# Performance work log

Measured on AMD Instinct MI355X. Metric: run time of the kernel, lower is better.

Reference implementation:

```python
import jax, jax.numpy as jnp
import numpy as np

D_MODEL, D_K, D_V, H, D_FF = 512, 64, 64, 8, 2048
B, N = 8, 1024
LN_EPS = 1e-5


def _layer_norm(x, g, b):
    mu = jnp.mean(x, axis=-1, keepdims=True)
    var = jnp.mean((x - mu) ** 2, axis=-1, keepdims=True)
    return (x - mu) * jax.lax.rsqrt(var + LN_EPS) * g + b


def setup_inputs() -> dict:
    key = jax.random.key(0)
    ks = jax.random.split(key, 16)
    s = 0.02
    return {
        "queries": jax.random.normal(ks[0], (B, N, D_MODEL), jnp.float32),
        "keys": jax.random.normal(ks[1], (B, N, D_MODEL), jnp.float32),
        "values": jax.random.normal(ks[2], (B, N, D_MODEL), jnp.float32),
        "relative_geometry_weights": jax.random.uniform(ks[3], (B, H, N, N), jnp.float32),
        "pos": jax.random.normal(ks[4], (B, N, D_MODEL), jnp.float32),
        "Wq": jax.random.normal(ks[5], (D_MODEL, H * D_K), jnp.float32) * s,
        "bq": jnp.zeros((H * D_K,), jnp.float32),
        "Wk": jax.random.normal(ks[6], (D_MODEL, H * D_K), jnp.float32) * s,
        "bk": jnp.zeros((H * D_K,), jnp.float32),
        "Wv": jax.random.normal(ks[7], (D_MODEL, H * D_V), jnp.float32) * s,
        "bv": jnp.zeros((H * D_V,), jnp.float32),
        "Wo": jax.random.normal(ks[8], (H * D_V, D_MODEL), jnp.float32) * s,
        "bo": jnp.zeros((D_MODEL,), jnp.float32),
        "ln1_g": jnp.ones((D_MODEL,), jnp.float32),
        "ln1_b": jnp.zeros((D_MODEL,), jnp.float32),
        "W1": jax.random.normal(ks[9], (D_MODEL, D_FF), jnp.float32) * s,
        "b1": jnp.zeros((D_FF,), jnp.float32),
        "W2": jax.random.normal(ks[10], (D_FF, D_MODEL), jnp.float32) * s,
        "b2": jnp.zeros((D_MODEL,), jnp.float32),
        "ln2_g": jnp.ones((D_MODEL,), jnp.float32),
        "ln2_b": jnp.zeros((D_MODEL,), jnp.float32),
    }


def reference(queries, keys, values, relative_geometry_weights, pos,
              Wq, bq, Wk, bk, Wv, bv, Wo, bo, ln1_g, ln1_b,
              W1, b1, W2, b2, ln2_g, ln2_b):
    b, n, _ = queries.shape
    # positional injection on q/k only
    q_in = queries + pos
    k_in = keys + pos
    # projections -> [b, h, n, d]
    q = (q_in @ Wq + bq).reshape(b, n, H, D_K).transpose(0, 2, 1, 3)
    k = (k_in @ Wk + bk).reshape(b, n, H, D_K).transpose(0, 2, 1, 3)
    v = (values @ Wv + bv).reshape(b, n, H, D_V).transpose(0, 2, 1, 3)
    # scaled dot-product scores with geometry bias: log(clamp(w_g)) + scores
    att = jnp.einsum('bhqd,bhkd->bhqk', q, k) / jnp.sqrt(jnp.float32(D_K))
    w_mn = jnp.log(jnp.clip(relative_geometry_weights, 1e-6, None)) + att
    w_mn = jax.nn.softmax(w_mn, axis=-1)
    out = jnp.einsum('bhqk,bhkd->bhqd', w_mn, v)  # [b,h,n,d_v]
    out = out.transpose(0, 2, 1, 3).reshape(b, n, H * D_V) @ Wo + bo
    # residual + layernorm (dropout is identity in eval)
    att_out = _layer_norm(queries + out, ln1_g, ln1_b)
    # position-wise FFN with residual + layernorm
    ff = jax.nn.relu(att_out @ W1 + b1) @ W2 + b2
    return _layer_norm(att_out + ff, ln2_g, ln2_b)
```

## Files before the change

kernel.cpp:

```cpp
#include <hip/hip_runtime.h>
#include <hip/hip_bf16.h>
#include <stdint.h>

#define B_   8
#define N_   1024
#define DM   512
#define H_   8
#define DFF  2048
#define ROWS (B_ * N_)
#define QKV_LD (3 * DM)
#define LOG2E 1.4426950408889634f
#define SCL  (0.125f * LOG2E)

typedef __bf16 bf16x8 __attribute__((ext_vector_type(8)));
typedef float  f32x4  __attribute__((ext_vector_type(4)));

__device__ __forceinline__ void gld_lds16(const void* g, void* l) {
  __builtin_amdgcn_global_load_lds((__attribute__((address_space(1))) void*)g,
                                   (__attribute__((address_space(3))) void*)l, 16, 0, 0);
}

__device__ __forceinline__ unsigned short bfb(float x) {
  __bf16 h = (__bf16)x;
  unsigned short u;
  __builtin_memcpy(&u, &h, 2);
  return u;
}

__global__ __launch_bounds__(256) void prep_x(
    const float* __restrict__ q, const float* __restrict__ k,
    const float* __restrict__ v, const float* __restrict__ pos,
    __bf16* __restrict__ xq, __bf16* __restrict__ xk, __bf16* __restrict__ xv) {
  int i = blockIdx.x * 256 + threadIdx.x;
  float4 pv = ((const float4*)pos)[i];
  float4 qv = ((const float4*)q)[i];
  float4 kv = ((const float4*)k)[i];
  float4 vv = ((const float4*)v)[i];
  ushort4 o;
  o.x = bfb(qv.x + pv.x); o.y = bfb(qv.y + pv.y); o.z = bfb(qv.z + pv.z); o.w = bfb(qv.w + pv.w);
  ((ushort4*)xq)[i] = o;
  o.x = bfb(kv.x + pv.x); o.y = bfb(kv.y + pv.y); o.z = bfb(kv.z + pv.z); o.w = bfb(kv.w + pv.w);
  ((ushort4*)xk)[i] = o;
  o.x = bfb(vv.x); o.y = bfb(vv.y); o.z = bfb(vv.z); o.w = bfb(vv.w);
  ((ushort4*)xv)[i] = o;
}

__global__ __launch_bounds__(256) void transpose_all(
    const float* __restrict__ Wq, const float* __restrict__ Wk,
    const float* __restrict__ Wv, const float* __restrict__ Wo,
    const float* __restrict__ W1, const float* __restrict__ W2,
    __bf16* __restrict__ WqkvT, __bf16* __restrict__ WoT,
    __bf16* __restrict__ W1T, __bf16* __restrict__ W2T) {
  __shared__ float tl[32][33];
  int idx = blockIdx.x;
  const float* src; __bf16* dst; int K, N, t;
  if (idx < 768) {
    src = idx < 256 ? Wq : (idx < 512 ? Wk : Wv);
    dst = WqkvT + (size_t)(idx >> 8) * 512 * 512;
    K = 512; N = 512; t = idx & 255;
  } else if (idx < 1024) { src = Wo; dst = WoT;  K = 512;  N = 512;  t = idx - 768; }
  else if (idx < 2048)   { src = W1; dst = W1T;  K = 512;  N = 2048; t = idx - 1024; }
  else                   { src = W2; dst = W2T;  K = 2048; N = 512;  t = idx - 2048; }
  int tiles_n = N >> 5;
  int tn = t & (tiles_n - 1), tk = t / tiles_n;
  int n0 = tn * 32, k0 = tk * 32;
  int x = threadIdx.x & 31, y4 = threadIdx.x >> 5;
  #pragma unroll
  for (int j = y4; j < 32; j += 8) tl[j][x] = src[(size_t)(k0 + j) * N + n0 + x];
  __syncthreads();
  #pragma unroll
  for (int j = y4; j < 32; j += 8)
    dst[(size_t)(n0 + j) * K + k0 + x] = (__bf16)tl[x][j];
}

__global__ __launch_bounds__(256) void transpose_v(
    const __bf16* __restrict__ QKV, __bf16* __restrict__ Vt) {
  __shared__ __bf16 t[32][33];
  int bh = blockIdx.y;
  int b = bh >> 3, h = bh & 7;
  int tn = blockIdx.x >> 1;
  int td = blockIdx.x & 1;
  int x = threadIdx.x & 31, y4 = threadIdx.x >> 5;
  #pragma unroll
  for (int j = y4; j < 32; j += 8)
    t[j][x] = QKV[(size_t)(b * N_ + tn * 32 + j) * QKV_LD + 2 * DM + h * 64 + td * 32 + x];
  __syncthreads();
  #pragma unroll
  for (int j = y4; j < 32; j += 8)
    Vt[(size_t)(bh * 64 + td * 32 + j) * N_ + tn * 32 + x] = t[x][j];
}

template <int EPI, int BN>
__global__ __launch_bounds__(256, 2) void gemm_bt(
    const __bf16* __restrict__ A0, const __bf16* __restrict__ A1, const __bf16* __restrict__ A2,
    const __bf16* __restrict__ BT,
    const float* __restrict__ bias0, const float* __restrict__ bias1, const float* __restrict__ bias2,
    void* __restrict__ Cp, int M, int N, int K, int nsplit) {
  constexpr int NFR = BN / 32;
  constexpr int WCW = BN / 2;
  constexpr int BI  = BN / 32;
  __shared__ __align__(16) __bf16 As[128 * 64];
  __shared__ __align__(16) __bf16 Bs[BN * 64];
  int tid = threadIdx.x, lane = tid & 63;
  int wave = tid >> 6;
  int wr = (wave >> 1) * 64, wc = (wave & 1) * WCW;

  int gx = N / BN;
  int nwg = gridDim.x;
  int cpx = nwg >> 3;
  int swz = (blockIdx.x & 7) * cpx + (blockIdx.x >> 3);
  int bx = swz % gx, by = swz / gx;
  int row0 = by << 7, col0 = bx * BN;

  int asel = col0 / nsplit;
  const __bf16* A = asel == 0 ? A0 : (asel == 1 ? A1 : A2);
  const float* bias = asel == 0 ? bias0 : (asel == 1 ? bias1 : bias2);

  f32x4 acc[4][NFR] = {};

  for (int kt = 0; kt < K; kt += 64) {
    #pragma unroll
    for (int i = 0; i < 4; ++i) {
      int t = i * 256 + tid;
      int r = t >> 3, cL = t & 7;
      int cS = cL ^ (r & 7);
      gld_lds16(A + (size_t)(row0 + r) * K + kt + cS * 8, As + t * 8);
    }
    #pragma unroll
    for (int i = 0; i < BI; ++i) {
      int t = i * 256 + tid;
      int r = t >> 3, cL = t & 7;
      int cS = cL ^ (r & 7);
      gld_lds16(BT + (size_t)(col0 + r) * K + kt + cS * 8, Bs + t * 8);
    }
    __syncthreads();
    #pragma unroll
    for (int ks = 0; ks < 2; ++ks) {
      bf16x8 af[4], bfr[NFR];
      #pragma unroll
      for (int m = 0; m < 4; ++m) {
        int r = wr + m * 16 + (lane & 15);
        int c = (ks * 4 + (lane >> 4)) ^ (r & 7);
        af[m] = *(const bf16x8*)(As + r * 64 + c * 8);
      }
      #pragma unroll
      for (int n = 0; n < NFR; ++n) {
        int r = wc + n * 16 + (lane & 15);
        int c = (ks * 4 + (lane >> 4)) ^ (r & 7);
        bfr[n] = *(const bf16x8*)(Bs + r * 64 + c * 8);
      }
      #pragma unroll
      for (int m = 0; m < 4; ++m)
        #pragma unroll
        for (int n = 0; n < NFR; ++n)
          acc[m][n] = __builtin_amdgcn_mfma_f32_16x16x32_bf16(af[m], bfr[n], acc[m][n], 0, 0, 0);
    }
    __syncthreads();
  }

  int rb = row0 + wr + ((lane >> 4) << 2);
  int cb = col0 + wc + (lane & 15);
  #pragma unroll
  for (int n = 0; n < NFR; ++n) {
    int c = cb + n * 16;
    float bv = bias[c % nsplit];
    #pragma unroll
    for (int m = 0; m < 4; ++m) {
      #pragma unroll
      for (int j = 0; j < 4; ++j) {
        int r = rb + m * 16 + j;
        float v = acc[m][n][j] + bv;
        if (EPI == 1) v = fmaxf(v, 0.f);
        if (EPI == 2) ((float*)Cp)[(size_t)r * N + c] = v;
        else          ((__bf16*)Cp)[(size_t)r * N + c] = (__bf16)v;
      }
    }
  }
}

__global__ __launch_bounds__(256, 3) void attn_kernel(
    const __bf16* __restrict__ QKV, const __bf16* __restrict__ Vt,
    const float* __restrict__ rgw, __bf16* __restrict__ O) {
  __shared__ __align__(16) __bf16 Qs[64 * 64];
  __shared__ __align__(16) __bf16 Ks[2][64 * 64];
  __shared__ __align__(16) __bf16 Vs[2][64 * 64];
  __shared__ __align__(16) __bf16 Ps[4][16 * 64];

  int tid = threadIdx.x, lane = tid & 63, wave = tid >> 6;
  int flat = (blockIdx.x & 7) * 128 + (blockIdx.x >> 3);
  int qt = flat & 15, h = (flat >> 4) & 7, b = flat >> 7;
  int q0 = qt * 64;
  const int g = lane >> 4, u = lane & 15;

  const float* rgw_p = rgw +
      ((size_t)(b * H_ + h) * N_ + (size_t)(q0 + wave * 16 + u)) * N_ + g * 4;

#define STAGE_KV(BUF, KT)                                                      \
  {                                                                            \
    _Pragma("unroll")                                                          \
    for (int i = 0; i < 2; ++i) {                                              \
      int t = i * 256 + tid;                                                   \
      int r = t >> 3, cL = t & 7, cS = cL ^ (r & 7);                           \
      gld_lds16(QKV + (size_t)(b * N_ + (KT) + r) * QKV_LD + DM + h * 64 + cS * 8, Ks[BUF] + t * 8); \
      gld_lds16(Vt + (size_t)((b * H_ + h) * 64 + r) * N_ + (KT) + cS * 8, Vs[BUF] + t * 8);         \
    }                                                                          \
  }

  #pragma unroll
  for (int i = 0; i < 2; ++i) {
    int t = i * 256 + tid;
    int r = t >> 3, cL = t & 7, cS = cL ^ (r & 7);
    gld_lds16(QKV + (size_t)(b * N_ + q0 + r) * QKV_LD + h * 64 + cS * 8, Qs + t * 8);
  }
  STAGE_KV(0, 0)
  __builtin_amdgcn_sched_barrier(0);
  f32x4 wA[4], wB[4];
  #pragma unroll
  for (int n = 0; n < 4; ++n) wA[n] = *(const f32x4*)(rgw_p + n * 16);
  #pragma unroll
  for (int n = 0; n < 4; ++n) wB[n] = *(const f32x4*)(rgw_p + 64 + n * 16);

  float l = 0.f;
  f32x4 oacc[4] = {};
  bf16x8 qf[2];
  __bf16* pw = &Ps[wave][0];

  union Pk { __bf16 h4[4]; unsigned long long q; };

#define PHASE(T16, CUR, WC, DOSTAGE, DOPF, WAITSTR)                            \
  {                                                                            \
    asm volatile(WAITSTR ::: "memory");                                        \
    __builtin_amdgcn_s_barrier();                                              \
    if (DOSTAGE) { STAGE_KV((CUR) ^ 1, ((T16) + 1) * 64) }                     \
    __builtin_amdgcn_sched_barrier(0);      \
    if ((T16) == 0) {                                                          \
      int r = wave * 16 + u;                                                   \
      _Pragma("unroll")                                                        \
      for (int ks = 0; ks < 2; ++ks) {                                         \
        int c = (ks * 4 + g) ^ (r & 7);                                        \
        qf[ks] = *(const bf16x8*)(Qs + r * 64 + c * 8);                        \
      }                                                                        \
    }                                                                          \
                        \
    f32x4 s[4] = {};                                                           \
    __builtin_amdgcn_s_setprio(1);                                             \
    _Pragma("unroll")                                                          \
    for (int ks = 0; ks < 2; ++ks) {                                           \
      _Pragma("unroll")                                                        \
      for (int n = 0; n < 4; ++n) {                                            \
        int r = n * 16 + u;                                                    \
        int c = (ks * 4 + g) ^ (r & 7);                                        \
        bf16x8 kf = *(const bf16x8*)(Ks[CUR] + r * 64 + c * 8);                \
        s[n] = __builtin_amdgcn_mfma_f32_16x16x32_bf16(kf, qf[ks], s[n], 0, 0, 0); \
      }                                                                        \
    }                                                                          \
    __builtin_amdgcn_s_setprio(0);                                             \
                           \
    _Pragma("unroll")                                                          \
    for (int n = 0; n < 4; ++n) {                                              \
      Pk pk;                                                                   \
      _Pragma("unroll")                                                        \
      for (int j = 0; j < 4; ++j) {                                            \
        float pv = fmaxf(WC[n][j], 1e-6f) * exp2f(s[n][j] * SCL);              \
        l += pv;                                                               \
        pk.h4[j] = (__bf16)pv;                                                 \
      }                                                                        \
      int bcol = 2 * n + (g >> 1);                                             \
      *(unsigned long long*)(pw + u * 64 + ((bcol ^ (u & 7)) << 3) + ((g & 1) << 2)) = pk.q; \
    }                                                                          \
    if (DOPF) {                                                                \
      _Pragma("unroll")                                                        \
      for (int n = 0; n < 4; ++n)                                              \
        WC[n] = *(const f32x4*)(rgw_p + ((T16) + 2) * 64 + n * 16);            \
    }                                                                          \
                                                               \
    __builtin_amdgcn_s_setprio(1);                                             \
    _Pragma("unroll")                                                          \
    for (int ks = 0; ks < 2; ++ks) {                                           \
      int cp = (ks * 4 + g) ^ (u & 7);                                         \
      bf16x8 pa = *(const bf16x8*)(pw + u * 64 + cp * 8);                      \
      _Pragma("unroll")                                                        \
      for (int n = 0; n < 4; ++n) {                                            \
        int r = n * 16 + u;                                                    \
        int c = (ks * 4 + g) ^ (r & 7);                                        \
        bf16x8 vb = *(const bf16x8*)(Vs[CUR] + r * 64 + c * 8);                \
        oacc[n] = __builtin_amdgcn_mfma_f32_16x16x32_bf16(pa, vb, oacc[n], 0, 0, 0); \
      }                                                                        \
    }                                                                          \
    __builtin_amdgcn_s_setprio(0);                                             \
  }

  PHASE(0, 0, wA, 1, 1, "s_waitcnt vmcnt(4)")
  PHASE(1, 1, wB, 1, 1, "s_waitcnt vmcnt(4)")
  #pragma unroll 1
  for (int tt = 1; tt < 7; ++tt) {
    int t2 = tt * 2;
    PHASE(t2, 0, wA, 1, 1, "s_waitcnt vmcnt(4)")
    PHASE((t2 + 1), 1, wB, 1, 1, "s_waitcnt vmcnt(4)")
  }
  PHASE(14, 0, wA, 1, 0, "s_waitcnt vmcnt(4)")
  PHASE(15, 1, wB, 0, 0, "s_waitcnt vmcnt(0)")
#undef PHASE
#undef STAGE_KV

  l += __shfl_xor(l, 16);
  l += __shfl_xor(l, 32);
  float linv[4];
  #pragma unroll
  for (int j = 0; j < 4; ++j)
    linv[j] = 1.f / __shfl(l, (lane & 48) | (g * 4 + j));

  int orow = b * N_ + q0 + wave * 16 + g * 4;
  int ocol = h * 64 + u;
  #pragma unroll
  for (int j = 0; j < 4; ++j)
    #pragma unroll
    for (int n = 0; n < 4; ++n)
      O[(size_t)(orow + j) * DM + ocol + n * 16] = (__bf16)(oacc[n][j] * linv[j]);
}

template <int WRITE_BF>
__global__ __launch_bounds__(256) void ln_kernel(
    const float* __restrict__ x1, const float* __restrict__ x2,
    const float* __restrict__ gw, const float* __restrict__ bw,
    float* __restrict__ outf, __bf16* __restrict__ outb) {
  __shared__ float red[8];
  int row = blockIdx.x, t = threadIdx.x;
  size_t base = (size_t)row * DM;
  float v0 = x1[base + t] + x2[base + t];
  float v1 = x1[base + t + 256] + x2[base + t + 256];
  float s = v0 + v1, s2 = v0 * v0 + v1 * v1;
  #pragma unroll
  for (int o = 32; o; o >>= 1) { s += __shfl_xor(s, o); s2 += __shfl_xor(s2, o); }
  int wave = t >> 6;
  if ((t & 63) == 0) { red[wave] = s; red[4 + wave] = s2; }
  __syncthreads();
  s = red[0] + red[1] + red[2] + red[3];
  s2 = red[4] + red[5] + red[6] + red[7];
  float mu = s * (1.f / DM);
  float var = s2 * (1.f / DM) - mu * mu;
  float rstd = rsqrtf(var + 1e-5f);
  float y0 = (v0 - mu) * rstd * gw[t] + bw[t];
  float y1 = (v1 - mu) * rstd * gw[t + 256] + bw[t + 256];
  outf[base + t] = y0;
  outf[base + t + 256] = y1;
  if (WRITE_BF) {
    outb[base + t] = (__bf16)y0;
    outb[base + t + 256] = (__bf16)y1;
  }
}

extern "C" void kernel_launch(void* const* d_in, const int* in_sizes, int n_in,
                              void* d_out, int out_size, void* d_ws, size_t ws_size,
                              hipStream_t stream) {
  const float* queries = (const float*)d_in[0];
  const float* keys    = (const float*)d_in[1];
  const float* values  = (const float*)d_in[2];
  const float* rgw     = (const float*)d_in[3];
  const float* pos     = (const float*)d_in[4];
  const float* Wq = (const float*)d_in[5];
  const float* bq = (const float*)d_in[6];
  const float* Wk = (const float*)d_in[7];
  const float* bk = (const float*)d_in[8];
  const float* Wv = (const float*)d_in[9];
  const float* bv = (const float*)d_in[10];
  const float* Wo = (const float*)d_in[11];
  const float* bo = (const float*)d_in[12];
  const float* ln1g = (const float*)d_in[13];
  const float* ln1b = (const float*)d_in[14];
  const float* W1 = (const float*)d_in[15];
  const float* b1 = (const float*)d_in[16];
  const float* W2 = (const float*)d_in[17];
  const float* b2 = (const float*)d_in[18];
  const float* ln2g = (const float*)d_in[19];
  const float* ln2b = (const float*)d_in[20];
  float* out = (float*)d_out;

  char* ws = (char*)d_ws;
  const size_t SZX = (size_t)ROWS * DM * 2;
  __bf16* Xq    = (__bf16*)(ws);
  __bf16* Xk    = (__bf16*)(ws + SZX);
  __bf16* Xv    = (__bf16*)(ws + 2 * SZX);
  __bf16* WqkvT = (__bf16*)(ws + 3 * SZX);
  __bf16* WoT   = (__bf16*)(ws + 3 * SZX + 1572864);
  __bf16* W1T   = (__bf16*)(ws + 3 * SZX + 2097152);
  __bf16* W2T   = (__bf16*)(ws + 3 * SZX + 4194304);
  __bf16* QKV   = (__bf16*)(ws + 3 * SZX + 6291456);
  __bf16* Vt    = (__bf16*)(ws + 3 * SZX + 6291456 + 3 * SZX);
  __bf16* Oat   = (__bf16*)(ws + 3 * SZX + 6291456 + 4 * SZX);
  __bf16* ff1   = (__bf16*)(ws + 3 * SZX + 6291456 + 5 * SZX);
  float*  attproj = (float*)Xq;
  __bf16* attoutb = Xv;
  float*  attoutf = (float*)QKV;
  float*  ff2     = (float*)Vt;

  prep_x<<<ROWS * DM / 4 / 256, 256, 0, stream>>>(queries, keys, values, pos, Xq, Xk, Xv);
  transpose_all<<<3072, 256, 0, stream>>>(Wq, Wk, Wv, Wo, W1, W2, WqkvT, WoT, W1T, W2T);

  gemm_bt<0, 128><<<(ROWS / 128) * (QKV_LD / 128), 256, 0, stream>>>(
      Xq, Xk, Xv, WqkvT, bq, bk, bv, QKV, ROWS, QKV_LD, DM, DM);

  transpose_v<<<dim3(64, B_ * H_), 256, 0, stream>>>(QKV, Vt);

  attn_kernel<<<B_ * H_ * (N_ / 64), 256, 0, stream>>>(QKV, Vt, rgw, Oat);

  gemm_bt<2, 64><<<(ROWS / 128) * (DM / 64), 256, 0, stream>>>(
      Oat, Oat, Oat, WoT, bo, bo, bo, attproj, ROWS, DM, DM, DM);

  ln_kernel<1><<<ROWS, 256, 0, stream>>>(queries, attproj, ln1g, ln1b, attoutf, attoutb);

  gemm_bt<1, 128><<<(ROWS / 128) * (DFF / 128), 256, 0, stream>>>(
      attoutb, attoutb, attoutb, W1T, b1, b1, b1, ff1, ROWS, DFF, DM, DFF);

  gemm_bt<2, 64><<<(ROWS / 128) * (DM / 64), 256, 0, stream>>>(
      ff1, ff1, ff1, W2T, b2, b2, b2, ff2, ROWS, DM, DFF, DM);

  ln_kernel<0><<<ROWS, 256, 0, stream>>>(attoutf, ff2, ln2g, ln2b, out, nullptr);
}
```

Measured before the change: 240.7 us.

## Fuse V transpose into QKV GEMM epilogue, merge prep kernels, deepen rgw prefetch

```diff
diff --git a/kernel.cpp b/kernel.cpp
--- a/kernel.cpp
+++ b/kernel.cpp
@@ -27,32 +27,32 @@
   return u;
 }
 
-__global__ __launch_bounds__(256) void prep_x(
+__global__ __launch_bounds__(256) void prep_and_wt(
     const float* __restrict__ q, const float* __restrict__ k,
     const float* __restrict__ v, const float* __restrict__ pos,
-    __bf16* __restrict__ xq, __bf16* __restrict__ xk, __bf16* __restrict__ xv) {
-  int i = blockIdx.x * 256 + threadIdx.x;
-  float4 pv = ((const float4*)pos)[i];
-  float4 qv = ((const float4*)q)[i];
-  float4 kv = ((const float4*)k)[i];
-  float4 vv = ((const float4*)v)[i];
-  ushort4 o;
-  o.x = bfb(qv.x + pv.x); o.y = bfb(qv.y + pv.y); o.z = bfb(qv.z + pv.z); o.w = bfb(qv.w + pv.w);
-  ((ushort4*)xq)[i] = o;
-  o.x = bfb(kv.x + pv.x); o.y = bfb(kv.y + pv.y); o.z = bfb(kv.z + pv.z); o.w = bfb(kv.w + pv.w);
-  ((ushort4*)xk)[i] = o;
-  o.x = bfb(vv.x); o.y = bfb(vv.y); o.z = bfb(vv.z); o.w = bfb(vv.w);
-  ((ushort4*)xv)[i] = o;
-}
-
-__global__ __launch_bounds__(256) void transpose_all(
+    __bf16* __restrict__ xq, __bf16* __restrict__ xk, __bf16* __restrict__ xv,
     const float* __restrict__ Wq, const float* __restrict__ Wk,
     const float* __restrict__ Wv, const float* __restrict__ Wo,
     const float* __restrict__ W1, const float* __restrict__ W2,
     __bf16* __restrict__ WqkvT, __bf16* __restrict__ WoT,
     __bf16* __restrict__ W1T, __bf16* __restrict__ W2T) {
   __shared__ float tl[32][33];
-  int idx = blockIdx.x;
+  if (blockIdx.x < 4096) {
+    int i = blockIdx.x * 256 + threadIdx.x;
+    float4 pv = ((const float4*)pos)[i];
+    float4 qv = ((const float4*)q)[i];
+    float4 kv = ((const float4*)k)[i];
+    float4 vv = ((const float4*)v)[i];
+    ushort4 o;
+    o.x = bfb(qv.x + pv.x); o.y = bfb(qv.y + pv.y); o.z = bfb(qv.z + pv.z); o.w = bfb(qv.w + pv.w);
+    ((ushort4*)xq)[i] = o;
+    o.x = bfb(kv.x + pv.x); o.y = bfb(kv.y + pv.y); o.z = bfb(kv.z + pv.z); o.w = bfb(kv.w + pv.w);
+    ((ushort4*)xk)[i] = o;
+    o.x = bfb(vv.x); o.y = bfb(vv.y); o.z = bfb(vv.z); o.w = bfb(vv.w);
+    ((ushort4*)xv)[i] = o;
+    return;
+  }
+  int idx = blockIdx.x - 4096;
   const float* src; __bf16* dst; int K, N, t;
   if (idx < 768) {
     src = idx < 256 ? Wq : (idx < 512 ? Wk : Wv);
@@ -73,29 +73,12 @@
     dst[(size_t)(n0 + j) * K + k0 + x] = (__bf16)tl[x][j];
 }
 
-__global__ __launch_bounds__(256) void transpose_v(
-    const __bf16* __restrict__ QKV, __bf16* __restrict__ Vt) {
-  __shared__ __bf16 t[32][33];
-  int bh = blockIdx.y;
-  int b = bh >> 3, h = bh & 7;
-  int tn = blockIdx.x >> 1;
-  int td = blockIdx.x & 1;
-  int x = threadIdx.x & 31, y4 = threadIdx.x >> 5;
-  #pragma unroll
-  for (int j = y4; j < 32; j += 8)
-    t[j][x] = QKV[(size_t)(b * N_ + tn * 32 + j) * QKV_LD + 2 * DM + h * 64 + td * 32 + x];
-  __syncthreads();
-  #pragma unroll
-  for (int j = y4; j < 32; j += 8)
-    Vt[(size_t)(bh * 64 + td * 32 + j) * N_ + tn * 32 + x] = t[x][j];
-}
-
 template <int EPI, int BN>
 __global__ __launch_bounds__(256, 2) void gemm_bt(
     const __bf16* __restrict__ A0, const __bf16* __restrict__ A1, const __bf16* __restrict__ A2,
     const __bf16* __restrict__ BT,
     const float* __restrict__ bias0, const float* __restrict__ bias1, const float* __restrict__ bias2,
-    void* __restrict__ Cp, int M, int N, int K, int nsplit) {
+    void* __restrict__ Cp, __bf16* __restrict__ Vtp, int M, int N, int K, int nsplit) {
   constexpr int NFR = BN / 32;
   constexpr int WCW = BN / 2;
   constexpr int BI  = BN / 32;
@@ -160,6 +143,27 @@
 
   int rb = row0 + wr + ((lane >> 4) << 2);
   int cb = col0 + wc + (lane & 15);
+  if (EPI == 3 && asel == 2) {
+    int bb = row0 >> 10;
+    #pragma unroll
+    for (int n = 0; n < NFR; ++n) {
+      int c = cb + n * 16;
+      int d = c & 63, hh = (c >> 6) & 7;
+      float bv = bias[c % nsplit];
+      size_t vbase = ((size_t)((bb * 8 + hh) * 64 + d)) << 10;
+      #pragma unroll
+      for (int m = 0; m < 4; ++m) {
+        int r0 = (rb + m * 16) & 1023;
+        ushort4 pk;
+        pk.x = bfb(acc[m][n][0] + bv);
+        pk.y = bfb(acc[m][n][1] + bv);
+        pk.z = bfb(acc[m][n][2] + bv);
+        pk.w = bfb(acc[m][n][3] + bv);
+        *(ushort4*)((__bf16*)Vtp + vbase + r0) = pk;
+      }
+    }
+    return;
+  }
   #pragma unroll
   for (int n = 0; n < NFR; ++n) {
     int c = cb + n * 16;
@@ -205,6 +209,12 @@
       gld_lds16(Vt + (size_t)((b * H_ + h) * 64 + r) * N_ + (KT) + cS * 8, Vs[BUF] + t * 8);         \
     }                                                                          \
   }
+#define RPF(W, T)                                                              \
+  {                                                                            \
+    _Pragma("unroll")                                                          \
+    for (int n = 0; n < 4; ++n)                                                \
+      W[n] = __builtin_nontemporal_load((const f32x4*)(rgw_p + (size_t)(T) * 64 + n * 16)); \
+  }
 
   #pragma unroll
   for (int i = 0; i < 2; ++i) {
@@ -214,11 +224,9 @@
   }
   STAGE_KV(0, 0)
   __builtin_amdgcn_sched_barrier(0);
-  f32x4 wA[4], wB[4];
-  #pragma unroll
-  for (int n = 0; n < 4; ++n) wA[n] = *(const f32x4*)(rgw_p + n * 16);
-  #pragma unroll
-  for (int n = 0; n < 4; ++n) wB[n] = *(const f32x4*)(rgw_p + 64 + n * 16);
+  f32x4 wA[4], wB[4], wC[4], wD[4];
+  RPF(wA, 0) RPF(wB, 1) RPF(wC, 2)
+  __builtin_amdgcn_sched_barrier(0);
 
   float l = 0.f;
   f32x4 oacc[4] = {};
@@ -227,12 +235,14 @@
 
   union Pk { __bf16 h4[4]; unsigned long long q; };
 
-#define PHASE(T16, CUR, WC, DOSTAGE, DOPF, WAITSTR)                            \
+#define PHASE(T16, WAITSTR, DOSTAGE, DORPF, WCON, WPF)                         \
   {                                                                            \
     asm volatile(WAITSTR ::: "memory");                                        \
     __builtin_amdgcn_s_barrier();                                              \
-    if (DOSTAGE) { STAGE_KV((CUR) ^ 1, ((T16) + 1) * 64) }                     \
-    __builtin_amdgcn_sched_barrier(0);      \
+    if (DOSTAGE) { STAGE_KV(((T16) + 1) & 1, ((T16) + 1) * 64) }               \
+    __builtin_amdgcn_sched_barrier(0);                                         \
+    if (DORPF) { RPF(WPF, (T16) + 3) }                                         \
+    __builtin_amdgcn_sched_barrier(0);                                         \
     if ((T16) == 0) {                                                          \
       int r = wave * 16 + u;                                                   \
       _Pragma("unroll")                                                        \
@@ -241,7 +251,6 @@
         qf[ks] = *(const bf16x8*)(Qs + r * 64 + c * 8);                        \
       }                                                                        \
     }                                                                          \
-                        \
     f32x4 s[4] = {};                                                           \
     __builtin_amdgcn_s_setprio(1);                                             \
     _Pragma("unroll")                                                          \
@@ -250,30 +259,23 @@
       for (int n = 0; n < 4; ++n) {                                            \
         int r = n * 16 + u;                                                    \
         int c = (ks * 4 + g) ^ (r & 7);                                        \
-        bf16x8 kf = *(const bf16x8*)(Ks[CUR] + r * 64 + c * 8);                \
+        bf16x8 kf = *(const bf16x8*)(Ks[(T16) & 1] + r * 64 + c * 8);          \
         s[n] = __builtin_amdgcn_mfma_f32_16x16x32_bf16(kf, qf[ks], s[n], 0, 0, 0); \
       }                                                                        \
     }                                                                          \
     __builtin_amdgcn_s_setprio(0);                                             \
-                           \
     _Pragma("unroll")                                                          \
     for (int n = 0; n < 4; ++n) {                                              \
       Pk pk;                                                                   \
       _Pragma("unroll")                                                        \
       for (int j = 0; j < 4; ++j) {                                            \
-        float pv = fmaxf(WC[n][j], 1e-6f) * exp2f(s[n][j] * SCL);              \
+        float pv = fmaxf(WCON[n][j], 1e-6f) * exp2f(s[n][j] * SCL);            \
         l += pv;                                                               \
         pk.h4[j] = (__bf16)pv;                                                 \
       }                                                                        \
       int bcol = 2 * n + (g >> 1);                                             \
       *(unsigned long long*)(pw + u * 64 + ((bcol ^ (u & 7)) << 3) + ((g & 1) << 2)) = pk.q; \
     }                                                                          \
-    if (DOPF) {                                                                \
-      _Pragma("unroll")                                                        \
-      for (int n = 0; n < 4; ++n)                                              \
-        WC[n] = *(const f32x4*)(rgw_p + ((T16) + 2) * 64 + n * 16);            \
-    }                                                                          \
-                                                               \
     __builtin_amdgcn_s_setprio(1);                                             \
     _Pragma("unroll")                                                          \
     for (int ks = 0; ks < 2; ++ks) {                                           \
@@ -283,25 +285,32 @@
       for (int n = 0; n < 4; ++n) {                                            \
         int r = n * 16 + u;                                                    \
         int c = (ks * 4 + g) ^ (r & 7);                                        \
-        bf16x8 vb = *(const bf16x8*)(Vs[CUR] + r * 64 + c * 8);                \
+        bf16x8 vb = *(const bf16x8*)(Vs[(T16) & 1] + r * 64 + c * 8);          \
         oacc[n] = __builtin_amdgcn_mfma_f32_16x16x32_bf16(pa, vb, oacc[n], 0, 0, 0); \
       }                                                                        \
     }                                                                          \
     __builtin_amdgcn_s_setprio(0);                                             \
   }
 
-  PHASE(0, 0, wA, 1, 1, "s_waitcnt vmcnt(4)")
-  PHASE(1, 1, wB, 1, 1, "s_waitcnt vmcnt(4)")
-  #pragma unroll 1
-  for (int tt = 1; tt < 7; ++tt) {
-    int t2 = tt * 2;
-    PHASE(t2, 0, wA, 1, 1, "s_waitcnt vmcnt(4)")
-    PHASE((t2 + 1), 1, wB, 1, 1, "s_waitcnt vmcnt(4)")
-  }
-  PHASE(14, 0, wA, 1, 0, "s_waitcnt vmcnt(4)")
-  PHASE(15, 1, wB, 0, 0, "s_waitcnt vmcnt(0)")
+  PHASE(0,  "s_waitcnt vmcnt(12)", 1, 1, wA, wD)
+  PHASE(1,  "s_waitcnt vmcnt(4)",  1, 1, wB, wA)
+  PHASE(2,  "s_waitcnt vmcnt(4)",  1, 1, wC, wB)
+  PHASE(3,  "s_waitcnt vmcnt(4)",  1, 1, wD, wC)
+  PHASE(4,  "s_waitcnt vmcnt(4)",  1, 1, wA, wD)
+  PHASE(5,  "s_waitcnt vmcnt(4)",  1, 1, wB, wA)
+  PHASE(6,  "s_waitcnt vmcnt(4)",  1, 1, wC, wB)
+  PHASE(7,  "s_waitcnt vmcnt(4)",  1, 1, wD, wC)
+  PHASE(8,  "s_waitcnt vmcnt(4)",  1, 1, wA, wD)
+  PHASE(9,  "s_waitcnt vmcnt(4)",  1, 1, wB, wA)
+  PHASE(10, "s_waitcnt vmcnt(4)",  1, 1, wC, wB)
+  PHASE(11, "s_waitcnt vmcnt(4)",  1, 1, wD, wC)
+  PHASE(12, "s_waitcnt vmcnt(4)",  1, 1, wA, wD)
+  PHASE(13, "s_waitcnt vmcnt(4)",  1, 0, wB, wA)
+  PHASE(14, "s_waitcnt vmcnt(0)",  1, 0, wC, wB)
+  PHASE(15, "s_waitcnt vmcnt(0)",  0, 0, wD, wC)
 #undef PHASE
 #undef STAGE_KV
+#undef RPF
 
   l += __shfl_xor(l, 16);
   l += __shfl_xor(l, 32);
@@ -388,32 +397,31 @@
   __bf16* QKV   = (__bf16*)(ws + 3 * SZX + 6291456);
   __bf16* Vt    = (__bf16*)(ws + 3 * SZX + 6291456 + 3 * SZX);
   __bf16* Oat   = (__bf16*)(ws + 3 * SZX + 6291456 + 4 * SZX);
-  __bf16* ff1   = (__bf16*)(ws + 3 * SZX + 6291456 + 5 * SZX);
   float*  attproj = (float*)Xq;
   __bf16* attoutb = Xv;
   float*  attoutf = (float*)QKV;
   float*  ff2     = (float*)Vt;
-
-  prep_x<<<ROWS * DM / 4 / 256, 256, 0, stream>>>(queries, keys, values, pos, Xq, Xk, Xv);
-  transpose_all<<<3072, 256, 0, stream>>>(Wq, Wk, Wv, Wo, W1, W2, WqkvT, WoT, W1T, W2T);
-
-  gemm_bt<0, 128><<<(ROWS / 128) * (QKV_LD / 128), 256, 0, stream>>>(
-      Xq, Xk, Xv, WqkvT, bq, bk, bv, QKV, ROWS, QKV_LD, DM, DM);
-
-  transpose_v<<<dim3(64, B_ * H_), 256, 0, stream>>>(QKV, Vt);
+  __bf16* ff1     = (__bf16*)(ws + 3 * SZX + 6291456 + 5 * SZX);
+
+  prep_and_wt<<<4096 + 3072, 256, 0, stream>>>(
+      queries, keys, values, pos, Xq, Xk, Xv,
+      Wq, Wk, Wv, Wo, W1, W2, WqkvT, WoT, W1T, W2T);
+
+  gemm_bt<3, 128><<<(ROWS / 128) * (QKV_LD / 128), 256, 0, stream>>>(
+      Xq, Xk, Xv, WqkvT, bq, bk, bv, QKV, Vt, ROWS, QKV_LD, DM, DM);
 
   attn_kernel<<<B_ * H_ * (N_ / 64), 256, 0, stream>>>(QKV, Vt, rgw, Oat);
 
   gemm_bt<2, 64><<<(ROWS / 128) * (DM / 64), 256, 0, stream>>>(
-      Oat, Oat, Oat, WoT, bo, bo, bo, attproj, ROWS, DM, DM, DM);
+      Oat, Oat, Oat, WoT, bo, bo, bo, attproj, nullptr, ROWS, DM, DM, DM);
 
   ln_kernel<1><<<ROWS, 256, 0, stream>>>(queries, attproj, ln1g, ln1b, attoutf, attoutb);
 
   gemm_bt<1, 128><<<(ROWS / 128) * (DFF / 128), 256, 0, stream>>>(
-      attoutb, attoutb, attoutb, W1T, b1, b1, b1, ff1, ROWS, DFF, DM, DFF);
+      attoutb, attoutb, attoutb, W1T, b1, b1, b1, ff1, nullptr, ROWS, DFF, DM, DFF);
 
   gemm_bt<2, 64><<<(ROWS / 128) * (DM / 64), 256, 0, stream>>>(
-      ff1, ff1, ff1, W2T, b2, b2, b2, ff2, ROWS, DM, DFF, DM);
+      ff1, ff1, ff1, W2T, b2, b2, b2, ff2, nullptr, ROWS, DM, DFF, DM);
 
   ln_kernel<0><<<ROWS, 256, 0, stream>>>(attoutf, ff2, ln2g, ln2b, out, nullptr);
 }
```

Result: faster. 223.6 us (-7.1%).
